# Performance work log

Hardware: AMD Instinct MI355X
Metric: run time of the kernel (lower is better)

## Reference

```python
import jax, jax.numpy as jnp
import numpy as np

B, V, F, H, L, FL, OUT = 128, 128, 40, 256, 32, 1024, 1
LN_EPS = 1e-5


def _uni(key, shape, fan_in):
    s = 1.0 / np.sqrt(fan_in)
    return jax.random.uniform(key, shape, jnp.float32, minval=-s, maxval=s)


def setup_inputs() -> dict:
    key = jax.random.key(0)
    ks = jax.random.split(key, 12)
    x = jax.random.normal(ks[0], (B, V, F), jnp.float32)
    # sparse-ish symmetric 0/1 adjacency with zero diagonal
    A = (jax.random.uniform(ks[1], (B, V, V)) < 0.08).astype(jnp.float32)
    A = jnp.triu(A, 1)
    G = A + jnp.swapaxes(A, 1, 2)
    return {
        "x": x,
        "G": G,
        "W_feat": _uni(ks[2], (F, H), F),
        "b_feat": _uni(ks[3], (H,), F),
        "W_layers": _uni(ks[4], (L, H, H), H),
        "b_layers": _uni(ks[5], (L, H), H),
        "ln_g": jnp.ones((H,), jnp.float32),
        "ln_b": jnp.zeros((H,), jnp.float32),
        "W_fin": _uni(ks[6], (H, FL), H),
        "b_fin": _uni(ks[7], (FL,), H),
        "W_out": _uni(ks[8], (FL, OUT), FL),
        "b_out": _uni(ks[9], (OUT,), FL),
    }


def reference(x, G, W_feat, b_feat, W_layers, b_layers, ln_g, ln_b, W_fin, b_fin, W_out, b_out):
    # vertex featurization: [B,V,F] -> [B,V,H]
    v = x @ W_feat + b_feat

    # degree correction: G' = G + diag(rowsum(G)) (einsum('ij,jk->ijk', n, eye))
    n = jnp.sum(G, axis=2)                                   # [B,V]
    eye = jnp.eye(V, dtype=G.dtype)
    Gp = G + n[..., None] * eye                              # [B,V,V]
    diag = jnp.diagonal(Gp, axis1=-2, axis2=-1)              # [B,V]
    deg = diag + (diag == 0).astype(diag.dtype)              # zero-protect

    def step(v, wb):
        W, b = wb
        vp = v @ W + b                                       # linear first (order=True)
        m = jnp.einsum('bij,bjd->bid', Gp, vp) / deg[..., None]  # mean message passing
        return v + jax.nn.relu(m), None                      # residual

    v, _ = jax.lax.scan(step, v, (W_layers, b_layers))

    # OutputLayer: LayerNorm -> Linear -> ReLU -> Linear
    mu = jnp.mean(v, axis=-1, keepdims=True)
    var = jnp.mean((v - mu) ** 2, axis=-1, keepdims=True)
    h = (v - mu) / jnp.sqrt(var + LN_EPS) * ln_g + ln_b
    h = jax.nn.relu(h @ W_fin + b_fin)
    return h @ W_out + b_out                                 # [B,V,1]
```

## Files before the change

kernel.cpp:

```cpp
#include <hip/hip_runtime.h>

#define Bsz 128
#define Vn  128
#define Fdim 40
#define Hdim 256
#define Lnum 32
#define FLdim 1024
#define LN_EPS 1e-5f

typedef unsigned short u16;
typedef __attribute__((ext_vector_type(8))) short short8;
typedef __attribute__((ext_vector_type(4))) float f32x4;

__device__ __forceinline__ u16 f2bf(float f) {
    unsigned u = __float_as_uint(f);
    u += 0x7fff + ((u >> 16) & 1);
    return (u16)(u >> 16);
}
__device__ __forceinline__ float bf2f(u16 s) {
    return __uint_as_float((unsigned)s << 16);
}

__device__ __forceinline__ void split4(const f32x4& f, ushort4& h4, ushort4& l4) {
    u16 h0 = f2bf(f[0]), h1 = f2bf(f[1]), h2 = f2bf(f[2]), h3 = f2bf(f[3]);
    h4.x = h0; h4.y = h1; h4.z = h2; h4.w = h3;
    l4.x = f2bf(f[0] - bf2f(h0));
    l4.y = f2bf(f[1] - bf2f(h1));
    l4.z = f2bf(f[2] - bf2f(h2));
    l4.w = f2bf(f[3] - bf2f(h3));
}

__global__ __launch_bounds__(256) void rowsum_kernel(const float* __restrict__ G,
                                                     float* __restrict__ nrow,
                                                     float* __restrict__ invdeg) {
    int row = blockIdx.x * 4 + (threadIdx.x >> 6);
    int lane = threadIdx.x & 63;
    const float* g = G + (size_t)row * Vn;
    float s = g[lane] + g[lane + 64];
    #pragma unroll
    for (int off = 32; off; off >>= 1) s += __shfl_down(s, off);
    if (lane == 0) {
        nrow[row] = s;
        invdeg[row] = 1.0f / (s + (s == 0.0f ? 1.0f : 0.0f));
    }
}

__global__ __launch_bounds__(256) void gbf_kernel(const float* __restrict__ G,
                                                  const float* __restrict__ nrow,
                                                  u16* __restrict__ gbf) {
    int gid = blockIdx.x * 256 + threadIdx.x;
    int j8 = gid & 15;
    int m  = gid >> 4;
    int i  = m & 127;
    const float* src = G + (size_t)m * Vn + j8 * 8;
    float4 g0 = *(const float4*)src;
    float4 g1 = *(const float4*)(src + 4);
    float nb = nrow[m];
    float ge[8] = {g0.x, g0.y, g0.z, g0.w, g1.x, g1.y, g1.z, g1.w};
    u16 us[8];
    #pragma unroll
    for (int e = 0; e < 8; ++e) {
        float val = ge[e] + ((j8 * 8 + e) == i ? nb : 0.0f);
        us[e] = f2bf(val);
    }
    uint4 pack;
    pack.x = (unsigned)us[0] | ((unsigned)us[1] << 16);
    pack.y = (unsigned)us[2] | ((unsigned)us[3] << 16);
    pack.z = (unsigned)us[4] | ((unsigned)us[5] << 16);
    pack.w = (unsigned)us[6] | ((unsigned)us[7] << 16);
    *(uint4*)(gbf + (size_t)m * Vn + j8 * 8) = pack;
}

__global__ __launch_bounds__(256) void tsplit_kernel(const float* __restrict__ src,
                                                     u16* __restrict__ hi, u16* __restrict__ lo,
                                                     int N, int K) {
    __shared__ float tl[64][65];
    size_t mat = (size_t)blockIdx.z * K * N;
    int k0 = blockIdx.x * 64, n0 = blockIdx.y * 64;
    int t = threadIdx.x, c = t & 63, r4 = t >> 6;
    #pragma unroll
    for (int i = 0; i < 16; ++i) {
        int r = i * 4 + r4;
        tl[r][c] = src[mat + (size_t)(k0 + r) * N + n0 + c];
    }
    __syncthreads();
    #pragma unroll
    for (int i = 0; i < 16; ++i) {
        int nr = i * 4 + r4;
        float val = tl[c][nr];
        u16 h = f2bf(val);
        size_t idx = mat + (size_t)(n0 + nr) * K + k0 + c;
        hi[idx] = h;
        lo[idx] = f2bf(val - bf2f(h));
    }
}

__global__ __launch_bounds__(256) void feat_kernel(const float* __restrict__ x,
                                                   const float* __restrict__ Wf,
                                                   const float* __restrict__ bf,
                                                   float* __restrict__ v) {
    __shared__ float xs[Fdim];
    int row = blockIdx.x;
    int h = threadIdx.x;
    if (h < Fdim) xs[h] = x[(size_t)row * Fdim + h];
    __syncthreads();
    float acc = bf[h];
    #pragma unroll 8
    for (int f = 0; f < Fdim; ++f) acc += xs[f] * Wf[f * Hdim + h];
    v[(size_t)row * Hdim + h] = acc;
}

__global__ __launch_bounds__(512, 2) void layers_all(float* __restrict__ v_io,
                                                     const u16* __restrict__ wthi_all,
                                                     const u16* __restrict__ wtlo_all,
                                                     const float* __restrict__ b_all,
                                                     const u16* __restrict__ gbf,
                                                     const float* __restrict__ invdeg) {
    extern __shared__ char smem[];
    char* AsH = smem;
    char* AsL = smem + 65536;
    char* VPH = smem;
    char* VPL = smem + 65536;

    const int tid = threadIdx.x, l = tid & 63, w = tid >> 6;
    const int wr = w >> 2, wc = w & 3;
    const int b = blockIdx.x;
    const int lr = l & 15, lq = l >> 4, lkb = lq * 16;
    const int sw = (lr & 7) << 4;

    const char* gb = (const char*)gbf + (size_t)b * 32768;
    short8 gfr[2][4];
    #pragma unroll
    for (int ni = 0; ni < 2; ++ni)
        #pragma unroll
        for (int kc = 0; kc < 4; ++kc)
            gfr[ni][kc] = *(const short8*)(gb + (size_t)(wc * 32 + ni * 16 + lr) * 256 + kc * 64 + lkb);

    float invd[2];
    #pragma unroll
    for (int ni = 0; ni < 2; ++ni) invd[ni] = invdeg[b * 128 + wc * 32 + ni * 16 + lr];

    float* vb = v_io + (size_t)b * 128 * 256;
    f32x4 vreg[2][4][2];
    #pragma unroll
    for (int dd = 0; dd < 2; ++dd)
        #pragma unroll
        for (int mi = 0; mi < 4; ++mi)
            #pragma unroll
            for (int ni = 0; ni < 2; ++ni) {
                int i = wc * 32 + ni * 16 + lr;
                int d0 = dd * 128 + wr * 64 + mi * 16 + lq * 4;
                vreg[dd][mi][ni] = *(const f32x4*)(vb + (size_t)i * 256 + d0);
            }

    for (int layer = 0; layer < Lnum; ++layer) {
        const char* wh = (const char*)wthi_all + (size_t)layer * 131072;
        const char* wl_ = (const char*)wtlo_all + (size_t)layer * 131072;
        const float* bias = b_all + layer * 256;
        float bv[2][2];
        #pragma unroll
        for (int dd = 0; dd < 2; ++dd)
            #pragma unroll
            for (int ni = 0; ni < 2; ++ni)
                bv[dd][ni] = bias[dd * 128 + wc * 32 + ni * 16 + lr];

        __syncthreads();
        #pragma unroll
        for (int dd = 0; dd < 2; ++dd)
            #pragma unroll
            for (int mi = 0; mi < 4; ++mi)
                #pragma unroll
                for (int ni = 0; ni < 2; ++ni) {
                    int i = wc * 32 + ni * 16 + lr;
                    int d0 = dd * 128 + wr * 64 + mi * 16 + lq * 4;
                    ushort4 h4, l4;
                    split4(vreg[dd][mi][ni], h4, l4);
                    int off = (i * 512 + d0 * 2) ^ sw;
                    *(ushort4*)(AsH + off) = h4;
                    *(ushort4*)(AsL + off) = l4;
                }
        __syncthreads();

        f32x4 z = {0.f, 0.f, 0.f, 0.f};
        f32x4 acc1[2][4][2];
        #pragma unroll
        for (int dd = 0; dd < 2; ++dd)
            #pragma unroll
            for (int mi = 0; mi < 4; ++mi) { acc1[dd][mi][0] = z; acc1[dd][mi][1] = z; }

        #pragma unroll 2
        for (int kc = 0; kc < 8; ++kc) {
            short8 Bh[2][2], Bl[2][2];
            #pragma unroll
            for (int dd = 0; dd < 2; ++dd)
                #pragma unroll
                for (int ni = 0; ni < 2; ++ni) {
                    size_t woff = (size_t)(dd * 128 + wc * 32 + ni * 16 + lr) * 512 + kc * 64 + lkb;
                    Bh[dd][ni] = *(const short8*)(wh + woff);
                    Bl[dd][ni] = *(const short8*)(wl_ + woff);
                }
            short8 Ah[4], Al[4];
            #pragma unroll
            for (int mi = 0; mi < 4; ++mi) {
                int off = ((wr * 64 + mi * 16 + lr) * 512 + kc * 64 + lkb) ^ sw;
                Ah[mi] = *(const short8*)(AsH + off);
                Al[mi] = *(const short8*)(AsL + off);
            }
            #pragma unroll
            for (int dd = 0; dd < 2; ++dd)
                #pragma unroll
                for (int mi = 0; mi < 4; ++mi)
                    #pragma unroll
                    for (int ni = 0; ni < 2; ++ni) {
                        acc1[dd][mi][ni] = __builtin_amdgcn_mfma_f32_16x16x32_bf16(
                            Ah[mi], Bh[dd][ni], acc1[dd][mi][ni], 0, 0, 0);
                        acc1[dd][mi][ni] = __builtin_amdgcn_mfma_f32_16x16x32_bf16(
                            Al[mi], Bh[dd][ni], acc1[dd][mi][ni], 0, 0, 0);
                        acc1[dd][mi][ni] = __builtin_amdgcn_mfma_f32_16x16x32_bf16(
                            Ah[mi], Bl[dd][ni], acc1[dd][mi][ni], 0, 0, 0);
                    }
        }
        __syncthreads();

        #pragma unroll
        for (int dd = 0; dd < 2; ++dd)
            #pragma unroll
            for (int mi = 0; mi < 4; ++mi)
                #pragma unroll
                for (int ni = 0; ni < 2; ++ni) {
                    int d = dd * 128 + wc * 32 + ni * 16 + lr;
                    int j0 = wr * 64 + mi * 16 + lq * 4;
                    f32x4 t = acc1[dd][mi][ni];
                    t[0] += bv[dd][ni]; t[1] += bv[dd][ni];
                    t[2] += bv[dd][ni]; t[3] += bv[dd][ni];
                    ushort4 h4, l4;
                    split4(t, h4, l4);
                    int off = (d * 256 + j0 * 2) ^ sw;
                    *(ushort4*)(VPH + off) = h4;
                    *(ushort4*)(VPL + off) = l4;
                }
        __syncthreads();

        f32x4 acc2[2][4][2];
        #pragma unroll
        for (int dd = 0; dd < 2; ++dd)
            #pragma unroll
            for (int mi = 0; mi < 4; ++mi) { acc2[dd][mi][0] = z; acc2[dd][mi][1] = z; }

        #pragma unroll
        for (int s = 0; s < 2; ++s) {
            const char* Aseg = s ? VPL : VPH;
            #pragma unroll
            for (int kc = 0; kc < 4; ++kc) {
                short8 Af[2][4];
                #pragma unroll
                for (int dd = 0; dd < 2; ++dd)
                    #pragma unroll
                    for (int mi = 0; mi < 4; ++mi) {
                        int off = ((dd * 128 + wr * 64 + mi * 16 + lr) * 256 + kc * 64 + lkb) ^ sw;
                        Af[dd][mi] = *(const short8*)(Aseg + off);
                    }
                #pragma unroll
                for (int dd = 0; dd < 2; ++dd)
                    #pragma unroll
                    for (int mi = 0; mi < 4; ++mi)
                        #pragma unroll
                        for (int ni = 0; ni < 2; ++ni)
                            acc2[dd][mi][ni] = __builtin_amdgcn_mfma_f32_16x16x32_bf16(
                                Af[dd][mi], gfr[ni][kc], acc2[dd][mi][ni], 0, 0, 0);
            }
        }

        #pragma unroll
        for (int dd = 0; dd < 2; ++dd)
            #pragma unroll
            for (int mi = 0; mi < 4; ++mi)
                #pragma unroll
                for (int ni = 0; ni < 2; ++ni)
                    #pragma unroll
                    for (int r = 0; r < 4; ++r)
                        vreg[dd][mi][ni][r] += fmaxf(acc2[dd][mi][ni][r] * invd[ni], 0.0f);
    }

    #pragma unroll
    for (int dd = 0; dd < 2; ++dd)
        #pragma unroll
        for (int mi = 0; mi < 4; ++mi)
            #pragma unroll
            for (int ni = 0; ni < 2; ++ni) {
                int i = wc * 32 + ni * 16 + lr;
                int d0 = dd * 128 + wr * 64 + mi * 16 + lq * 4;
                *(f32x4*)(vb + (size_t)i * 256 + d0) = vreg[dd][mi][ni];
            }
}

__global__ __launch_bounds__(256) void ln_kernel(const float* __restrict__ v,
                                                 const float* __restrict__ g,
                                                 const float* __restrict__ beta,
                                                 u16* __restrict__ hhi,
                                                 u16* __restrict__ hlo) {
    __shared__ float sbuf[4];
    int row = blockIdx.x;
    int t = threadIdx.x;
    float x = v[(size_t)row * Hdim + t];
    float s = x;
    #pragma unroll
    for (int off = 32; off; off >>= 1) s += __shfl_down(s, off);
    int wid = t >> 6, lane = t & 63;
    if (lane == 0) sbuf[wid] = s;
    __syncthreads();
    float mu = (sbuf[0] + sbuf[1] + sbuf[2] + sbuf[3]) * (1.0f / Hdim);
    __syncthreads();
    float d = x - mu;
    float sq = d * d;
    #pragma unroll
    for (int off = 32; off; off >>= 1) sq += __shfl_down(sq, off);
    if (lane == 0) sbuf[wid] = sq;
    __syncthreads();
    float var = (sbuf[0] + sbuf[1] + sbuf[2] + sbuf[3]) * (1.0f / Hdim);
    float h = d * (1.0f / sqrtf(var + LN_EPS)) * g[t] + beta[t];
    size_t idx = (size_t)row * Hdim + t;
    u16 hb = f2bf(h);
    hhi[idx] = hb;
    hlo[idx] = f2bf(h - bf2f(hb));
}

__global__ __launch_bounds__(256) void gemm_fin_mfma(const u16* __restrict__ hhi,
                                                     const u16* __restrict__ hlo,
                                                     const u16* __restrict__ wfhi,
                                                     const u16* __restrict__ wflo,
                                                     const float* __restrict__ bfin,
                                                     const float* __restrict__ wout,
                                                     float* __restrict__ part) {
    __shared__ char smem[24576];
    char* As = smem;
    char* Bs = smem + 16384;
    int tid = threadIdx.x, l = tid & 63, w = tid >> 6, wr = w >> 1, wc = w & 1;
    int m0 = blockIdx.x * 128, n0 = blockIdx.y * 64;
    const int lr = l & 15, lq = l >> 4, lkb = lq * 16;
    const int sw = (lr & 7) << 4;
    const char* segA[3] = {(const char*)hhi, (const char*)hlo, (const char*)hhi};
    const char* segB[3] = {(const char*)wfhi, (const char*)wfhi, (const char*)wflo};
    f32x4 z = {0.f, 0.f, 0.f, 0.f};
    f32x4 acc[4][2];
    #pragma unroll
    for (int mi = 0; mi < 4; ++mi) { acc[mi][0] = z; acc[mi][1] = z; }

    for (int q = 0; q < 12; ++q) {
        const char* A = segA[q >> 2] + (size_t)m0 * 512 + (q & 3) * 128;
        const char* B = segB[q >> 2] + (size_t)n0 * 512 + (q & 3) * 128;
        #pragma unroll
        for (int u = 0; u < 4; ++u) {
            int off = (u * 256 + tid) * 16;
            int row = off >> 7;
            *(uint4*)(As + (off ^ ((row & 7) << 4))) =
                *(const uint4*)(A + (size_t)row * 512 + (off & 127));
        }
        #pragma unroll
        for (int u = 0; u < 2; ++u) {
            int off = (u * 256 + tid) * 16;
            int row = off >> 7;
            *(uint4*)(Bs + (off ^ ((row & 7) << 4))) =
                *(const uint4*)(B + (size_t)row * 512 + (off & 127));
        }
        __syncthreads();
        #pragma unroll
        for (int kk = 0; kk < 2; ++kk) {
            short8 a[4], b2[2];
            #pragma unroll
            for (int mi = 0; mi < 4; ++mi)
                a[mi] = *(const short8*)(As + (((wr * 64 + mi * 16 + lr) * 128 + kk * 64 + lkb) ^ sw));
            #pragma unroll
            for (int ni = 0; ni < 2; ++ni)
                b2[ni] = *(const short8*)(Bs + (((wc * 32 + ni * 16 + lr) * 128 + kk * 64 + lkb) ^ sw));
            #pragma unroll
            for (int mi = 0; mi < 4; ++mi)
                #pragma unroll
                for (int ni = 0; ni < 2; ++ni)
                    acc[mi][ni] = __builtin_amdgcn_mfma_f32_16x16x32_bf16(a[mi], b2[ni],
                                                                         acc[mi][ni], 0, 0, 0);
        }
        __syncthreads();
    }
    float rs[4][4];
    #pragma unroll
    for (int mi = 0; mi < 4; ++mi)
        #pragma unroll
        for (int r = 0; r < 4; ++r) rs[mi][r] = 0.0f;
    #pragma unroll
    for (int ni = 0; ni < 2; ++ni) {
        int n = n0 + wc * 32 + ni * 16 + lr;
        float bvv = bfin[n], wo = wout[n];
        #pragma unroll
        for (int mi = 0; mi < 4; ++mi)
            #pragma unroll
            for (int r = 0; r < 4; ++r)
                rs[mi][r] += fmaxf(acc[mi][ni][r] + bvv, 0.0f) * wo;
    }
    float* red = (float*)smem;
    #pragma unroll
    for (int mi = 0; mi < 4; ++mi)
        #pragma unroll
        for (int r = 0; r < 4; ++r) {
            int row = wr * 64 + mi * 16 + lq * 4 + r;
            red[row * 33 + wc * 16 + lr] = rs[mi][r];
        }
    __syncthreads();
    if (tid < 128) {
        float s = 0.0f;
        #pragma unroll
        for (int c = 0; c < 32; ++c) s += red[tid * 33 + c];
        part[(size_t)(m0 + tid) * 16 + blockIdx.y] = s;
    }
}

__global__ __launch_bounds__(256) void final_kernel(const float* __restrict__ part,
                                                    const float* __restrict__ bo,
                                                    float* __restrict__ out) {
    int i = blockIdx.x * 256 + threadIdx.x;
    float s = bo[0];
    #pragma unroll
    for (int t = 0; t < 16; ++t) s += part[(size_t)i * 16 + t];
    out[i] = s;
}

extern "C" void kernel_launch(void* const* d_in, const int* in_sizes, int n_in,
                              void* d_out, int out_size, void* d_ws, size_t ws_size,
                              hipStream_t stream) {
    const float* x        = (const float*)d_in[0];
    const float* G        = (const float*)d_in[1];
    const float* W_feat   = (const float*)d_in[2];
    const float* b_feat   = (const float*)d_in[3];
    const float* W_layers = (const float*)d_in[4];
    const float* b_layers = (const float*)d_in[5];
    const float* ln_g     = (const float*)d_in[6];
    const float* ln_b     = (const float*)d_in[7];
    const float* W_fin    = (const float*)d_in[8];
    const float* b_fin    = (const float*)d_in[9];
    const float* W_out    = (const float*)d_in[10];
    const float* b_out    = (const float*)d_in[11];
    float* out = (float*)d_out;

    const int M = Bsz * Vn;
    char* ws = (char*)d_ws;
    float* v0     = (float*)ws;                      ws += (size_t)M * Hdim * 4;
    u16*   gbf    = (u16*)ws;                        ws += (size_t)Bsz * Vn * Vn * 2;
    u16*   wthi   = (u16*)ws;                        ws += (size_t)Lnum * Hdim * Hdim * 2;
    u16*   wtlo   = (u16*)ws;                        ws += (size_t)Lnum * Hdim * Hdim * 2;
    u16*   wfhi   = (u16*)ws;                        ws += (size_t)FLdim * Hdim * 2;
    u16*   wflo   = (u16*)ws;                        ws += (size_t)FLdim * Hdim * 2;
    float* nrow   = (float*)ws;                      ws += (size_t)M * 4;
    float* invdeg = (float*)ws;                      ws += (size_t)M * 4;
    float* part   = (float*)ws;                      ws += (size_t)M * 16 * 4;
    u16*   hh     = (u16*)ws;                        ws += (size_t)M * Hdim * 2;
    u16*   hl     = (u16*)ws;                        ws += (size_t)M * Hdim * 2;

    hipFuncSetAttribute((const void*)layers_all,
                        hipFuncAttributeMaxDynamicSharedMemorySize, 131072);

    rowsum_kernel<<<M / 4, 256, 0, stream>>>(G, nrow, invdeg);
    gbf_kernel<<<(Bsz * Vn * 16) / 256, 256, 0, stream>>>(G, nrow, gbf);
    tsplit_kernel<<<dim3(4, 4, Lnum), 256, 0, stream>>>(W_layers, wthi, wtlo, Hdim, Hdim);
    tsplit_kernel<<<dim3(4, 16, 1), 256, 0, stream>>>(W_fin, wfhi, wflo, FLdim, Hdim);
    feat_kernel<<<M, 256, 0, stream>>>(x, W_feat, b_feat, v0);

    layers_all<<<Bsz, 512, 131072, stream>>>(v0, wthi, wtlo, b_layers, gbf, invdeg);

    ln_kernel<<<M, 256, 0, stream>>>(v0, ln_g, ln_b, hh, hl);
    gemm_fin_mfma<<<dim3(M / 128, FLdim / 64), 256, 0, stream>>>(
        hh, hl, wfhi, wflo, b_fin, W_out, part);
    final_kernel<<<M / 256, 256, 0, stream>>>(part, b_out, out);
}
```

Baseline: 872.8 us.

## Remap wave tiling in fused layer kernel to cut weight fetches per wave

Changes the 8-wave decomposition of the per-graph layer kernel from a 2x4 grid to 2 column halves by 4 row quarters. In the linear GEMM each wave now covers 32 rows and 128 output features, so it loads 8 weight fragment pairs per k-chunk instead of 4 and only 2 A fragment pairs instead of 4, which shifts work from LDS reads to global weight reads. The LDS swizzle widens from 8 to 16 rows to fit the new access pattern. Register layout of the residual state and accumulators is reshaped to match, so register pressure and global weight traffic may change.

```diff
diff --git a/kernel.cpp b/kernel.cpp
--- a/kernel.cpp
+++ b/kernel.cpp
@@ -123,10 +123,10 @@
     char* VPL = smem + 65536;
 
     const int tid = threadIdx.x, l = tid & 63, w = tid >> 6;
-    const int wr = w >> 2, wc = w & 3;
+    const int wlo = w & 1, whi = w >> 1;
     const int b = blockIdx.x;
-    const int lr = l & 15, lq = l >> 4, lkb = lq * 16;
-    const int sw = (lr & 7) << 4;
+    const int lr = l & 15, lq = l >> 4;
+    const int sw = lr << 4;
 
     const char* gb = (const char*)gbf + (size_t)b * 32768;
     short8 gfr[2][4];
@@ -134,164 +134,136 @@
     for (int ni = 0; ni < 2; ++ni)
         #pragma unroll
         for (int kc = 0; kc < 4; ++kc)
-            gfr[ni][kc] = *(const short8*)(gb + (size_t)(wc * 32 + ni * 16 + lr) * 256 + kc * 64 + lkb);
+            gfr[ni][kc] = *(const short8*)(gb + (size_t)(whi * 32 + ni * 16 + lr) * 256 + kc * 64 + lq * 16);
 
     float invd[2];
     #pragma unroll
-    for (int ni = 0; ni < 2; ++ni) invd[ni] = invdeg[b * 128 + wc * 32 + ni * 16 + lr];
+    for (int ni = 0; ni < 2; ++ni) invd[ni] = invdeg[b * 128 + whi * 32 + ni * 16 + lr];
 
     float* vb = v_io + (size_t)b * 128 * 256;
-    f32x4 vreg[2][4][2];
-    #pragma unroll
-    for (int dd = 0; dd < 2; ++dd)
-        #pragma unroll
-        for (int mi = 0; mi < 4; ++mi)
-            #pragma unroll
-            for (int ni = 0; ni < 2; ++ni) {
-                int i = wc * 32 + ni * 16 + lr;
-                int d0 = dd * 128 + wr * 64 + mi * 16 + lq * 4;
-                vreg[dd][mi][ni] = *(const f32x4*)(vb + (size_t)i * 256 + d0);
-            }
+    f32x4 vreg[8][2];
+    #pragma unroll
+    for (int mi = 0; mi < 8; ++mi)
+        #pragma unroll
+        for (int ni = 0; ni < 2; ++ni) {
+            int i = whi * 32 + ni * 16 + lr;
+            int d0 = wlo * 128 + mi * 16 + lq * 4;
+            vreg[mi][ni] = *(const f32x4*)(vb + (size_t)i * 256 + d0);
+        }
 
     for (int layer = 0; layer < Lnum; ++layer) {
         const char* wh = (const char*)wthi_all + (size_t)layer * 131072;
         const char* wl_ = (const char*)wtlo_all + (size_t)layer * 131072;
         const float* bias = b_all + layer * 256;
-        float bv[2][2];
-        #pragma unroll
-        for (int dd = 0; dd < 2; ++dd)
-            #pragma unroll
-            for (int ni = 0; ni < 2; ++ni)
-                bv[dd][ni] = bias[dd * 128 + wc * 32 + ni * 16 + lr];
-
-        __syncthreads();
-        #pragma unroll
-        for (int dd = 0; dd < 2; ++dd)
-            #pragma unroll
-            for (int mi = 0; mi < 4; ++mi)
-                #pragma unroll
-                for (int ni = 0; ni < 2; ++ni) {
-                    int i = wc * 32 + ni * 16 + lr;
-                    int d0 = dd * 128 + wr * 64 + mi * 16 + lq * 4;
-                    ushort4 h4, l4;
-                    split4(vreg[dd][mi][ni], h4, l4);
-                    int off = (i * 512 + d0 * 2) ^ sw;
-                    *(ushort4*)(AsH + off) = h4;
-                    *(ushort4*)(AsL + off) = l4;
-                }
+        float bv1[8];
+        #pragma unroll
+        for (int bn = 0; bn < 8; ++bn)
+            bv1[bn] = bias[wlo * 128 + bn * 16 + lr];
+
+        __syncthreads();
+        #pragma unroll
+        for (int mi = 0; mi < 8; ++mi)
+            #pragma unroll
+            for (int ni = 0; ni < 2; ++ni) {
+                int j = whi * 32 + ni * 16 + lr;
+                int kb = wlo * 256 + mi * 32 + lq * 8;
+                ushort4 h4, l4;
+                split4(vreg[mi][ni], h4, l4);
+                int off = (j * 512 + kb) ^ sw;
+                *(ushort4*)(AsH + off) = h4;
+                *(ushort4*)(AsL + off) = l4;
+            }
         __syncthreads();
 
         f32x4 z = {0.f, 0.f, 0.f, 0.f};
-        f32x4 acc1[2][4][2];
-        #pragma unroll
-        for (int dd = 0; dd < 2; ++dd)
-            #pragma unroll
-            for (int mi = 0; mi < 4; ++mi) { acc1[dd][mi][0] = z; acc1[dd][mi][1] = z; }
+        f32x4 acc1[2][8];
+        #pragma unroll
+        for (int am = 0; am < 2; ++am)
+            #pragma unroll
+            for (int bn = 0; bn < 8; ++bn) acc1[am][bn] = z;
 
         #pragma unroll 2
         for (int kc = 0; kc < 8; ++kc) {
-            short8 Bh[2][2], Bl[2][2];
-            #pragma unroll
-            for (int dd = 0; dd < 2; ++dd)
+            short8 Ah[2], Al[2];
+            #pragma unroll
+            for (int am = 0; am < 2; ++am) {
+                int off = ((whi * 32 + am * 16 + lr) * 512 + kc * 64 + lq * 16) ^ sw;
+                Ah[am] = *(const short8*)(AsH + off);
+                Al[am] = *(const short8*)(AsL + off);
+            }
+            #pragma unroll
+            for (int bn = 0; bn < 8; ++bn) {
+                size_t woff = (size_t)(wlo * 128 + bn * 16 + lr) * 512 + kc * 64 + lq * 16;
+                short8 Bh = *(const short8*)(wh + woff);
+                short8 Bl = *(const short8*)(wl_ + woff);
                 #pragma unroll
-                for (int ni = 0; ni < 2; ++ni) {
-                    size_t woff = (size_t)(dd * 128 + wc * 32 + ni * 16 + lr) * 512 + kc * 64 + lkb;
-                    Bh[dd][ni] = *(const short8*)(wh + woff);
-                    Bl[dd][ni] = *(const short8*)(wl_ + woff);
+                for (int am = 0; am < 2; ++am) {
+                    acc1[am][bn] = __builtin_amdgcn_mfma_f32_16x16x32_bf16(Ah[am], Bh, acc1[am][bn], 0, 0, 0);
+                    acc1[am][bn] = __builtin_amdgcn_mfma_f32_16x16x32_bf16(Al[am], Bh, acc1[am][bn], 0, 0, 0);
+                    acc1[am][bn] = __builtin_amdgcn_mfma_f32_16x16x32_bf16(Ah[am], Bl, acc1[am][bn], 0, 0, 0);
                 }
-            short8 Ah[4], Al[4];
-            #pragma unroll
-            for (int mi = 0; mi < 4; ++mi) {
-                int off = ((wr * 64 + mi * 16 + lr) * 512 + kc * 64 + lkb) ^ sw;
-                Ah[mi] = *(const short8*)(AsH + off);
-                Al[mi] = *(const short8*)(AsL + off);
             }
-            #pragma unroll
-            for (int dd = 0; dd < 2; ++dd)
-                #pragma unroll
-                for (int mi = 0; mi < 4; ++mi)
-                    #pragma unroll
-                    for (int ni = 0; ni < 2; ++ni) {
-                        acc1[dd][mi][ni] = __builtin_amdgcn_mfma_f32_16x16x32_bf16(
-                            Ah[mi], Bh[dd][ni], acc1[dd][mi][ni], 0, 0, 0);
-                        acc1[dd][mi][ni] = __builtin_amdgcn_mfma_f32_16x16x32_bf16(
-                            Al[mi], Bh[dd][ni], acc1[dd][mi][ni], 0, 0, 0);
-                        acc1[dd][mi][ni] = __builtin_amdgcn_mfma_f32_16x16x32_bf16(
-                            Ah[mi], Bl[dd][ni], acc1[dd][mi][ni], 0, 0, 0);
-                    }
-        }
-        __syncthreads();
-
-        #pragma unroll
-        for (int dd = 0; dd < 2; ++dd)
-            #pragma unroll
-            for (int mi = 0; mi < 4; ++mi)
-                #pragma unroll
-                for (int ni = 0; ni < 2; ++ni) {
-                    int d = dd * 128 + wc * 32 + ni * 16 + lr;
-                    int j0 = wr * 64 + mi * 16 + lq * 4;
-                    f32x4 t = acc1[dd][mi][ni];
-                    t[0] += bv[dd][ni]; t[1] += bv[dd][ni];
-                    t[2] += bv[dd][ni]; t[3] += bv[dd][ni];
-                    ushort4 h4, l4;
-                    split4(t, h4, l4);
-                    int off = (d * 256 + j0 * 2) ^ sw;
-                    *(ushort4*)(VPH + off) = h4;
-                    *(ushort4*)(VPL + off) = l4;
-                }
-        __syncthreads();
-
-        f32x4 acc2[2][4][2];
-        #pragma unroll
-        for (int dd = 0; dd < 2; ++dd)
-            #pragma unroll
-            for (int mi = 0; mi < 4; ++mi) { acc2[dd][mi][0] = z; acc2[dd][mi][1] = z; }
+        }
+        __syncthreads();
+
+        #pragma unroll
+        for (int am = 0; am < 2; ++am)
+            #pragma unroll
+            for (int bn = 0; bn < 8; ++bn) {
+                int d = wlo * 128 + bn * 16 + lr;
+                int j0 = whi * 32 + am * 16 + lq * 4;
+                f32x4 t = acc1[am][bn];
+                t[0] += bv1[bn]; t[1] += bv1[bn];
+                t[2] += bv1[bn]; t[3] += bv1[bn];
+                ushort4 h4, l4;
+                split4(t, h4, l4);
+                int off = (d * 256 + j0 * 2) ^ sw;
+                *(ushort4*)(VPH + off) = h4;
+                *(ushort4*)(VPL + off) = l4;
+            }
+        __syncthreads();
+
+        f32x4 acc2[8][2];
+        #pragma unroll
+        for (int mi = 0; mi < 8; ++mi) { acc2[mi][0] = z; acc2[mi][1] = z; }
 
         #pragma unroll
         for (int s = 0; s < 2; ++s) {
             const char* Aseg = s ? VPL : VPH;
             #pragma unroll
             for (int kc = 0; kc < 4; ++kc) {
-                short8 Af[2][4];
+                short8 Af[8];
                 #pragma unroll
-                for (int dd = 0; dd < 2; ++dd)
+                for (int mi = 0; mi < 8; ++mi) {
+                    int off = ((wlo * 128 + mi * 16 + lr) * 256 + kc * 64 + lq * 16) ^ sw;
+                    Af[mi] = *(const short8*)(Aseg + off);
+                }
+                #pragma unroll
+                for (int mi = 0; mi < 8; ++mi)
                     #pragma unroll
-                    for (int mi = 0; mi < 4; ++mi) {
-                        int off = ((dd * 128 + wr * 64 + mi * 16 + lr) * 256 + kc * 64 + lkb) ^ sw;
-                        Af[dd][mi] = *(const short8*)(Aseg + off);
-                    }
+                    for (int ni = 0; ni < 2; ++ni)
+                        acc2[mi][ni] = __builtin_amdgcn_mfma_f32_16x16x32_bf16(
+                            Af[mi], gfr[ni][kc], acc2[mi][ni], 0, 0, 0);
+            }
+        }
+
+        #pragma unroll
+        for (int mi = 0; mi < 8; ++mi)
+            #pragma unroll
+            for (int ni = 0; ni < 2; ++ni)
                 #pragma unroll
-                for (int dd = 0; dd < 2; ++dd)
-                    #pragma unroll
-                    for (int mi = 0; mi < 4; ++mi)
-                        #pragma unroll
-                        for (int ni = 0; ni < 2; ++ni)
-                            acc2[dd][mi][ni] = __builtin_amdgcn_mfma_f32_16x16x32_bf16(
-                                Af[dd][mi], gfr[ni][kc], acc2[dd][mi][ni], 0, 0, 0);
-            }
-        }
-
-        #pragma unroll
-        for (int dd = 0; dd < 2; ++dd)
-            #pragma unroll
-            for (int mi = 0; mi < 4; ++mi)
-                #pragma unroll
-                for (int ni = 0; ni < 2; ++ni)
-                    #pragma unroll
-                    for (int r = 0; r < 4; ++r)
-                        vreg[dd][mi][ni][r] += fmaxf(acc2[dd][mi][ni][r] * invd[ni], 0.0f);
-    }
-
-    #pragma unroll
-    for (int dd = 0; dd < 2; ++dd)
-        #pragma unroll
-        for (int mi = 0; mi < 4; ++mi)
-            #pragma unroll
-            for (int ni = 0; ni < 2; ++ni) {
-                int i = wc * 32 + ni * 16 + lr;
-                int d0 = dd * 128 + wr * 64 + mi * 16 + lq * 4;
-                *(f32x4*)(vb + (size_t)i * 256 + d0) = vreg[dd][mi][ni];
-            }
+                for (int r = 0; r < 4; ++r)
+                    vreg[mi][ni][r] += fmaxf(acc2[mi][ni][r] * invd[ni], 0.0f);
+    }
+
+    #pragma unroll
+    for (int mi = 0; mi < 8; ++mi)
+        #pragma unroll
+        for (int ni = 0; ni < 2; ++ni) {
+            int i = whi * 32 + ni * 16 + lr;
+            int d0 = wlo * 128 + mi * 16 + lq * 4;
+            *(f32x4*)(vb + (size_t)i * 256 + d0) = vreg[mi][ni];
+        }
 }
 
 __global__ __launch_bounds__(256) void ln_kernel(const float* __restrict__ v,
```

Measured after the change: 1.345 ms. 54.1% more time.
